# Performance work log

Hardware: AMD Instinct MI355X
Metric: run time of the kernel (lower is better)

Reference implementation:

```python
import jax, jax.numpy as jnp
import numpy as np

FPS = [32, 64, 128, 256]
SPATIAL = [(32, 32, 32), (16, 16, 16), (8, 8, 8), (4, 4, 4)]
N_FEAT = 512
B = 2
HEAD_DIM = 16
EPS = 1e-5


def setup_inputs() -> dict:
    key = jax.random.key(0)
    ks = iter(jax.random.split(key, 64))
    inp = {}
    for i, (c, (h, w, z)) in enumerate(zip(FPS, SPATIAL)):
        inp[f"x{i}"] = jax.random.normal(next(ks), (B, c, h, w, z), jnp.float32)
        inp[f"f{i}"] = jax.random.normal(next(ks), (N_FEAT, c), jnp.float32)
        inp[f"kv_w{i}"] = jax.random.normal(next(ks), (2 * c, c), jnp.float32) * 0.02
        inp[f"kv_b{i}"] = jnp.zeros((2 * c,), jnp.float32)
        inp[f"proj_w{i}"] = jax.random.normal(next(ks), (c, c), jnp.float32) * 0.02
        inp[f"proj_b{i}"] = jnp.zeros((c,), jnp.float32)
        inp[f"ln_g{i}"] = jnp.ones((c,), jnp.float32)
        inp[f"ln_b{i}"] = jnp.zeros((c,), jnp.float32)
    inp["x4"] = jax.random.normal(next(ks), (B, 320, 2, 2, 2), jnp.float32)
    inp["x5"] = jax.random.normal(next(ks), (B, 320, 1, 1, 1), jnp.float32)
    return inp


def _block(x5d, feat, kv_w, kv_b, proj_w, proj_b, ln_g, ln_b):
    b, c, h, w, z = x5d.shape
    n = h * w * z
    H = c // HEAD_DIM
    # torch's x.view(b, h*w*z, c) is a raw reshape of [b,c,h,w,z] memory
    xq = x5d.reshape(b, n, c)
    N = feat.shape[0]
    f = jnp.broadcast_to(feat[None], (b, N, c))
    kv = f @ kv_w.T + kv_b                     # [b, N, 2c]
    kv = kv.reshape(b, N, 2, H, HEAD_DIM)
    k = kv[:, :, 0].transpose(0, 2, 1, 3)      # [b, H, N, hd]
    v = kv[:, :, 1].transpose(0, 2, 1, 3)      # [b, H, N, hd]
    q = xq.reshape(b, n, H, HEAD_DIM).transpose(0, 2, 1, 3) * (HEAD_DIM ** -0.5)
    attn = jax.nn.softmax(jnp.einsum('bhnd,bhmd->bhnm', q, k), axis=-1)
    o = jnp.einsum('bhnm,bhmd->bhnd', attn, v)
    o = o.transpose(0, 2, 1, 3).reshape(b, n, c)
    o = o @ proj_w.T + proj_b
    y = 0.5 * o + 0.5 * xq
    mu = jnp.mean(y, axis=-1, keepdims=True)
    var = jnp.var(y, axis=-1, keepdims=True)
    y = (y - mu) / jnp.sqrt(var + EPS) * ln_g + ln_b
    return y.reshape(b, c, h, w, z)


def reference(x0, x1, x2, x3, x4, x5, f0, f1, f2, f3,
              kv_w0, kv_b0, proj_w0, proj_b0, ln_g0, ln_b0,
              kv_w1, kv_b1, proj_w1, proj_b1, ln_g1, ln_b1,
              kv_w2, kv_b2, proj_w2, proj_b2, ln_g2, ln_b2,
              kv_w3, kv_b3, proj_w3, proj_b3, ln_g3, ln_b3):
    xs = [x0, x1, x2, x3]
    fs = [f0, f1, f2, f3]
    ps = [(kv_w0, kv_b0, proj_w0, proj_b0, ln_g0, ln_b0),
          (kv_w1, kv_b1, proj_w1, proj_b1, ln_g1, ln_b1),
          (kv_w2, kv_b2, proj_w2, proj_b2, ln_g2, ln_b2),
          (kv_w3, kv_b3, proj_w3, proj_b3, ln_g3, ln_b3)]
    res = [_block(xs[i], fs[i], *ps[i]) for i in range(4)]
    res.append(x4)  # stage 4: i >= 4 -> passthrough
    res.append(x5)  # last stage appended as-is
    return tuple(res)
```

## Files before the change

### kernel.cpp

```cpp
#include <hip/hip_runtime.h>

#define LOG2E 1.44269504088896340736f

struct Params {
  const float* x[4]; const float* f[4]; const float* kvw[4]; const float* kvb[4];
  const float* pw[4]; const float* pb[4]; const float* g[4]; const float* lb[4];
  float* kb[4]; float* vb[4]; float* ob[4]; float* out[4];
};

__device__ inline float dot4(float4 a, float4 b) {
  return fmaf(a.w, b.w, fmaf(a.z, b.z, fmaf(a.y, b.y, a.x * b.x)));
}
__device__ inline void fma4(float4& a, float p, float4 v) {
  a.x = fmaf(p, v.x, a.x); a.y = fmaf(p, v.y, a.y);
  a.z = fmaf(p, v.z, a.z); a.w = fmaf(p, v.w, a.w);
}
__device__ inline void scale4(float4& a, float r) { a.x *= r; a.y *= r; a.z *= r; a.w *= r; }

__global__ __launch_bounds__(256) void kv_all(Params P) {
  int bid = blockIdx.x;
  int s, local;
  if (bid < 8)       { s = 0; local = bid; }
  else if (bid < 24) { s = 1; local = bid - 8; }
  else if (bid < 56) { s = 2; local = bid - 24; }
  else               { s = 3; local = bid - 56; }
  const int C = 32 << s;
  int nt = local & 7, jt = local >> 3;
  int n0 = nt * 64, j0 = jt * 64;
  const float* __restrict__ f = P.f[s];
  const float* __restrict__ w = P.kvw[s];
  __shared__ float fa[64][17];
  __shared__ float wb[64][17];
  int t = threadIdx.x;
  int ti = t & 15, tj = t >> 4;
  float acc[4][4];
  #pragma unroll
  for (int a = 0; a < 4; a++)
    #pragma unroll
    for (int b = 0; b < 4; b++) acc[a][b] = 0.f;

  for (int k0 = 0; k0 < C; k0 += 16) {
    __syncthreads();
    for (int i = t; i < 1024; i += 256) {
      int r = i >> 4, kk = i & 15;
      fa[r][kk] = f[(n0 + r) * C + k0 + kk];
      wb[r][kk] = w[(j0 + r) * C + k0 + kk];
    }
    __syncthreads();
    #pragma unroll
    for (int kk = 0; kk < 16; ++kk) {
      float av[4], bv[4];
      #pragma unroll
      for (int ii = 0; ii < 4; ii++) av[ii] = fa[ti * 4 + ii][kk];
      #pragma unroll
      for (int jj = 0; jj < 4; jj++) bv[jj] = wb[tj * 4 + jj][kk];
      #pragma unroll
      for (int ii = 0; ii < 4; ii++)
        #pragma unroll
        for (int jj = 0; jj < 4; jj++)
          acc[ii][jj] = fmaf(av[ii], bv[jj], acc[ii][jj]);
    }
  }
  const float* __restrict__ bias = P.kvb[s];
  float* kb = P.kb[s]; float* vb = P.vb[s];
  #pragma unroll
  for (int ii = 0; ii < 4; ii++) {
    int n = n0 + ti * 4 + ii;
    #pragma unroll
    for (int jj = 0; jj < 4; jj++) {
      int j = j0 + tj * 4 + jj;
      float val = acc[ii][jj] + bias[j];
      if (j < C) {
        kb[((j >> 4) * 512 + n) * 16 + (j & 15)] = val;
      } else {
        int j2 = j - C;
        vb[((j2 >> 4) * 512 + n) * 16 + (j2 & 15)] = val;
      }
    }
  }
}

template <int C, int H>
__device__ void attn_stage(const Params& P, int s, int local, float4* kvl) {
  constexpr int ROWS = 2 * ((C == 32) ? 32768 : (C == 64) ? 4096 : (C == 128) ? 512 : 64);
  int tile = local / H, head = local % H;
  const float4* __restrict__ kh = (const float4*)(P.kb[s] + head * 8192);
  const float4* __restrict__ vh = (const float4*)(P.vb[s] + head * 8192);
  int t = threadIdx.x;
  int row = tile * 256 + t;
  bool valid = row < ROWS;
  int rc = valid ? row : (ROWS - 1);

  const float* xr = P.x[s] + (size_t)rc * C + head * 16;
  float4 q0 = ((const float4*)xr)[0], q1 = ((const float4*)xr)[1],
         q2 = ((const float4*)xr)[2], q3 = ((const float4*)xr)[3];
  const float qs = 0.25f * LOG2E;
  scale4(q0, qs); scale4(q1, qs); scale4(q2, qs); scale4(q3, qs);

  float m = -1e30f, l = 0.f;
  float4 a0 = {0,0,0,0}, a1 = {0,0,0,0}, a2 = {0,0,0,0}, a3 = {0,0,0,0};

  float4 pk0 = kh[t], pk1 = kh[t + 256], pv0 = vh[t], pv1 = vh[t + 256];
  kvl[t] = pk0; kvl[t + 256] = pk1; kvl[512 + t] = pv0; kvl[512 + t + 256] = pv1;

  for (int c = 0; c < 4; ++c) {
    if (c < 3) {
      const float4* kp = kh + (c + 1) * 512;
      const float4* vp = vh + (c + 1) * 512;
      pk0 = kp[t]; pk1 = kp[t + 256]; pv0 = vp[t]; pv1 = vp[t + 256];
    }
    __syncthreads();
    #pragma unroll 2
    for (int key = 0; key < 128; ++key) {
      float4 k0 = kvl[key * 4 + 0], k1 = kvl[key * 4 + 1],
             k2 = kvl[key * 4 + 2], k3 = kvl[key * 4 + 3];
      float s0 = dot4(q0, k0), s1 = dot4(q1, k1), s2 = dot4(q2, k2), s3 = dot4(q3, k3);
      float sc = (s0 + s1) + (s2 + s3);
      if (__any(sc > m + 8.f)) {
        float mn = fmaxf(m, sc);
        float r = __builtin_amdgcn_exp2f(m - mn);
        l *= r;
        scale4(a0, r); scale4(a1, r); scale4(a2, r); scale4(a3, r);
        m = mn;
      }
      float p = __builtin_amdgcn_exp2f(sc - m);
      l += p;
      float4 v0 = kvl[512 + key * 4 + 0], v1 = kvl[512 + key * 4 + 1],
             v2 = kvl[512 + key * 4 + 2], v3 = kvl[512 + key * 4 + 3];
      fma4(a0, p, v0); fma4(a1, p, v1); fma4(a2, p, v2); fma4(a3, p, v3);
    }
    __syncthreads();
    if (c < 3) {
      kvl[t] = pk0; kvl[t + 256] = pk1; kvl[512 + t] = pv0; kvl[512 + t + 256] = pv1;
    }
  }
  if (valid) {
    float inv = 1.f / l;
    scale4(a0, inv); scale4(a1, inv); scale4(a2, inv); scale4(a3, inv);
    float* orow = P.ob[s] + (size_t)row * C + head * 16;
    ((float4*)orow)[0] = a0; ((float4*)orow)[1] = a1;
    ((float4*)orow)[2] = a2; ((float4*)orow)[3] = a3;
  }
}

__global__ __launch_bounds__(256, 4) void attn_all(Params P) {
  __shared__ float4 kvlds[1024];
  int bid = blockIdx.x;
  if (bid < 512)      attn_stage<32, 2>(P, 0, bid, kvlds);
  else if (bid < 640) attn_stage<64, 4>(P, 1, bid - 512, kvlds);
  else if (bid < 672) attn_stage<128, 8>(P, 2, bid - 640, kvlds);
  else                attn_stage<256, 16>(P, 3, bid - 672, kvlds);
}

template <int C>
__device__ void proj_stage(const Params& P, int s, int tile, float* olds) {
  constexpr int CP = C + 4;
  constexpr int R = 256 / C;
  constexpr int NR = 8;
  constexpr int RB = 2048 / C;
  int r0 = tile * RB;
  int t = threadIdx.x;
  const float4* __restrict__ obv = (const float4*)(P.ob[s] + (size_t)r0 * C);
  for (int i = t; i < 512; i += 256) {
    int row = i / (C / 4), kk = i % (C / 4);
    ((float4*)(olds + row * CP))[kk] = obv[i];
  }
  __syncthreads();
  int j = t % C, rg = t / C;
  const float* __restrict__ pw = P.pw[s];
  float acc[NR];
  #pragma unroll
  for (int i = 0; i < NR; ++i) acc[i] = 0.f;
  for (int k = 0; k < C; k += 4) {
    float4 w4 = *(const float4*)(pw + (size_t)j * C + k);
    #pragma unroll
    for (int i = 0; i < NR; ++i) {
      float4 o4 = *(const float4*)(olds + (rg + i * R) * CP + k);
      acc[i] = fmaf(o4.x, w4.x, acc[i]);
      acc[i] = fmaf(o4.y, w4.y, acc[i]);
      acc[i] = fmaf(o4.z, w4.z, acc[i]);
      acc[i] = fmaf(o4.w, w4.w, acc[i]);
    }
  }
  __syncthreads();
  float pbj = P.pb[s][j];
  const float* __restrict__ x = P.x[s];
  #pragma unroll
  for (int i = 0; i < NR; ++i) {
    int r = rg + i * R;
    float xv = x[(size_t)(r0 + r) * C + j];
    olds[r * CP + j] = 0.5f * (acc[i] + pbj) + 0.5f * xv;
  }
  __syncthreads();
  int lane = t & 63, wv = t >> 6;
  const float* __restrict__ g = P.g[s];
  const float* __restrict__ lb = P.lb[s];
  float* __restrict__ out = P.out[s];
  #pragma unroll
  for (int rr = 0; rr < RB / 4; ++rr) {
    int r = wv * (RB / 4) + rr;
    float sum = 0.f, sq = 0.f;
    #pragma unroll
    for (int ch = lane; ch < C; ch += 64) {
      float v = olds[r * CP + ch];
      sum += v; sq = fmaf(v, v, sq);
    }
    #pragma unroll
    for (int o = 32; o; o >>= 1) { sum += __shfl_xor(sum, o); sq += __shfl_xor(sq, o); }
    float mu = sum * (1.f / C);
    float var = sq * (1.f / C) - mu * mu;
    float rstd = rsqrtf(var + 1e-5f);
    #pragma unroll
    for (int ch = lane; ch < C; ch += 64) {
      float v = (olds[r * CP + ch] - mu) * rstd;
      out[(size_t)(r0 + r) * C + ch] = fmaf(v, g[ch], lb[ch]);
    }
  }
}

__global__ __launch_bounds__(256) void proj_ln_all(Params P) {
  __shared__ float olds[2304];
  int bid = blockIdx.x;
  if (bid < 1024)      proj_stage<32>(P, 0, bid, olds);
  else if (bid < 1280) proj_stage<64>(P, 1, bid - 1024, olds);
  else if (bid < 1344) proj_stage<128>(P, 2, bid - 1280, olds);
  else                 proj_stage<256>(P, 3, bid - 1344, olds);
}

extern "C" void kernel_launch(void* const* d_in, const int* in_sizes, int n_in,
                              void* d_out, int out_size, void* d_ws, size_t ws_size,
                              hipStream_t stream) {
  Params P;
  float* ws = (float*)d_ws;
  float* out = (float*)d_out;
  const size_t kvoff[4]  = {0, 32768, 98304, 229376};
  const size_t ksz[4]    = {16384, 32768, 65536, 131072};
  const size_t ooff[4]   = {491520, 2588672, 3112960, 3244032};
  const size_t outoff[4] = {0, 2097152, 2621440, 2752512};
  for (int i = 0; i < 4; ++i) {
    const int b = i * 8;
    P.x[i]   = (const float*)d_in[b + 0];
    P.f[i]   = (const float*)d_in[b + 1];
    P.kvw[i] = (const float*)d_in[b + 2];
    P.kvb[i] = (const float*)d_in[b + 3];
    P.pw[i]  = (const float*)d_in[b + 4];
    P.pb[i]  = (const float*)d_in[b + 5];
    P.g[i]   = (const float*)d_in[b + 6];
    P.lb[i]  = (const float*)d_in[b + 7];
    P.kb[i]  = ws + kvoff[i];
    P.vb[i]  = ws + kvoff[i] + ksz[i];
    P.ob[i]  = ws + ooff[i];
    P.out[i] = out + outoff[i];
  }
  hipMemcpyAsync(out + 2785280, d_in[32], 5120 * sizeof(float), hipMemcpyDeviceToDevice, stream);
  hipMemcpyAsync(out + 2790400, d_in[33], 640 * sizeof(float), hipMemcpyDeviceToDevice, stream);

  kv_all<<<120, 256, 0, stream>>>(P);
  attn_all<<<688, 256, 0, stream>>>(P);
  proj_ln_all<<<1360, 256, 0, stream>>>(P);
}
```

Measured before the change: 355.1 us.

## Process two query rows per thread with interleaved K/V layout in attention

The attention kernel now runs 128 threads per block, with each thread handling two query rows (row and row+128). Every K/V value read from shared memory is therefore reused for two rows. K and V are written interleaved per key (32 floats per key), so one shared-memory row holds both, and the math uses native vector types. The two memcpy calls for the passthrough tensors become one small copy kernel, saving an API call and a launch. In exchange, each thread holds more registers, there are fewer waves per block, and the online-softmax rescale is now evaluated jointly for both rows.

```diff
diff --git a/kernel.cpp b/kernel.cpp
--- a/kernel.cpp
+++ b/kernel.cpp
@@ -1,21 +1,16 @@
 #include <hip/hip_runtime.h>
 
 #define LOG2E 1.44269504088896340736f
+
+typedef float v4f __attribute__((ext_vector_type(4)));
 
 struct Params {
   const float* x[4]; const float* f[4]; const float* kvw[4]; const float* kvb[4];
   const float* pw[4]; const float* pb[4]; const float* g[4]; const float* lb[4];
-  float* kb[4]; float* vb[4]; float* ob[4]; float* out[4];
+  float* kb[4]; float* ob[4]; float* out[4];
 };
 
-__device__ inline float dot4(float4 a, float4 b) {
-  return fmaf(a.w, b.w, fmaf(a.z, b.z, fmaf(a.y, b.y, a.x * b.x)));
-}
-__device__ inline void fma4(float4& a, float p, float4 v) {
-  a.x = fmaf(p, v.x, a.x); a.y = fmaf(p, v.y, a.y);
-  a.z = fmaf(p, v.z, a.z); a.w = fmaf(p, v.w, a.w);
-}
-__device__ inline void scale4(float4& a, float r) { a.x *= r; a.y *= r; a.z *= r; a.w *= r; }
+__device__ inline v4f fmav(v4f a, v4f b, v4f c) { return a * b + c; }
 
 __global__ __launch_bounds__(256) void kv_all(Params P) {
   int bid = blockIdx.x;
@@ -62,7 +57,7 @@
     }
   }
   const float* __restrict__ bias = P.kvb[s];
-  float* kb = P.kb[s]; float* vb = P.vb[s];
+  float* kb = P.kb[s];
   #pragma unroll
   for (int ii = 0; ii < 4; ii++) {
     int n = n0 + ti * 4 + ii;
@@ -71,85 +66,106 @@
       int j = j0 + tj * 4 + jj;
       float val = acc[ii][jj] + bias[j];
       if (j < C) {
-        kb[((j >> 4) * 512 + n) * 16 + (j & 15)] = val;
+        kb[(j >> 4) * 16384 + n * 32 + (j & 15)] = val;
       } else {
         int j2 = j - C;
-        vb[((j2 >> 4) * 512 + n) * 16 + (j2 & 15)] = val;
+        kb[(j2 >> 4) * 16384 + n * 32 + 16 + (j2 & 15)] = val;
       }
     }
   }
 }
 
 template <int C, int H>
-__device__ void attn_stage(const Params& P, int s, int local, float4* kvl) {
+__device__ void attn_stage(const Params& P, int s, int local, v4f* kvl) {
   constexpr int ROWS = 2 * ((C == 32) ? 32768 : (C == 64) ? 4096 : (C == 128) ? 512 : 64);
   int tile = local / H, head = local % H;
-  const float4* __restrict__ kh = (const float4*)(P.kb[s] + head * 8192);
-  const float4* __restrict__ vh = (const float4*)(P.vb[s] + head * 8192);
+  const v4f* __restrict__ kvh = (const v4f*)(P.kb[s] + head * 16384);
   int t = threadIdx.x;
-  int row = tile * 256 + t;
-  bool valid = row < ROWS;
-  int rc = valid ? row : (ROWS - 1);
-
-  const float* xr = P.x[s] + (size_t)rc * C + head * 16;
-  float4 q0 = ((const float4*)xr)[0], q1 = ((const float4*)xr)[1],
-         q2 = ((const float4*)xr)[2], q3 = ((const float4*)xr)[3];
+  int rowA = tile * 256 + t, rowB = rowA + 128;
+  bool vA = rowA < ROWS, vB = rowB < ROWS;
+  int rA = vA ? rowA : (ROWS - 1), rB = vB ? rowB : (ROWS - 1);
+
+  const v4f* xa = (const v4f*)(P.x[s] + (size_t)rA * C + head * 16);
+  const v4f* xb = (const v4f*)(P.x[s] + (size_t)rB * C + head * 16);
   const float qs = 0.25f * LOG2E;
-  scale4(q0, qs); scale4(q1, qs); scale4(q2, qs); scale4(q3, qs);
-
-  float m = -1e30f, l = 0.f;
-  float4 a0 = {0,0,0,0}, a1 = {0,0,0,0}, a2 = {0,0,0,0}, a3 = {0,0,0,0};
-
-  float4 pk0 = kh[t], pk1 = kh[t + 256], pv0 = vh[t], pv1 = vh[t + 256];
-  kvl[t] = pk0; kvl[t + 256] = pk1; kvl[512 + t] = pv0; kvl[512 + t + 256] = pv1;
+  v4f qa0 = xa[0] * qs, qa1 = xa[1] * qs, qa2 = xa[2] * qs, qa3 = xa[3] * qs;
+  v4f qb0 = xb[0] * qs, qb1 = xb[1] * qs, qb2 = xb[2] * qs, qb3 = xb[3] * qs;
+
+  float ma = -1e30f, la = 0.f, mb = -1e30f, lb = 0.f;
+  v4f aa0 = 0.f, aa1 = 0.f, aa2 = 0.f, aa3 = 0.f;
+  v4f ab0 = 0.f, ab1 = 0.f, ab2 = 0.f, ab3 = 0.f;
+
+  v4f pk[8];
+  #pragma unroll
+  for (int j = 0; j < 8; ++j) pk[j] = kvh[t + 128 * j];
+  #pragma unroll
+  for (int j = 0; j < 8; ++j) kvl[t + 128 * j] = pk[j];
 
   for (int c = 0; c < 4; ++c) {
     if (c < 3) {
-      const float4* kp = kh + (c + 1) * 512;
-      const float4* vp = vh + (c + 1) * 512;
-      pk0 = kp[t]; pk1 = kp[t + 256]; pv0 = vp[t]; pv1 = vp[t + 256];
+      const v4f* src = kvh + (c + 1) * 1024;
+      #pragma unroll
+      for (int j = 0; j < 8; ++j) pk[j] = src[t + 128 * j];
     }
     __syncthreads();
     #pragma unroll 2
-    for (int key = 0; key < 128; ++key) {
-      float4 k0 = kvl[key * 4 + 0], k1 = kvl[key * 4 + 1],
-             k2 = kvl[key * 4 + 2], k3 = kvl[key * 4 + 3];
-      float s0 = dot4(q0, k0), s1 = dot4(q1, k1), s2 = dot4(q2, k2), s3 = dot4(q3, k3);
-      float sc = (s0 + s1) + (s2 + s3);
-      if (__any(sc > m + 8.f)) {
-        float mn = fmaxf(m, sc);
-        float r = __builtin_amdgcn_exp2f(m - mn);
-        l *= r;
-        scale4(a0, r); scale4(a1, r); scale4(a2, r); scale4(a3, r);
-        m = mn;
+    for (int kl = 0; kl < 128; ++kl) {
+      const v4f* row = kvl + kl * 8;
+      v4f k0 = row[0], k1 = row[1], k2 = row[2], k3 = row[3];
+      v4f ta = qa0 * k0; ta = fmav(qa1, k1, ta); ta = fmav(qa2, k2, ta); ta = fmav(qa3, k3, ta);
+      v4f tb = qb0 * k0; tb = fmav(qb1, k1, tb); tb = fmav(qb2, k2, tb); tb = fmav(qb3, k3, tb);
+      float sa = (ta.x + ta.y) + (ta.z + ta.w);
+      float sb = (tb.x + tb.y) + (tb.z + tb.w);
+      if (__any(fmaxf(sa - ma, sb - mb) > 8.f)) {
+        float mna = fmaxf(ma, sa);
+        float ra = __builtin_amdgcn_exp2f(ma - mna);
+        la *= ra; aa0 *= ra; aa1 *= ra; aa2 *= ra; aa3 *= ra; ma = mna;
+        float mnb = fmaxf(mb, sb);
+        float rb = __builtin_amdgcn_exp2f(mb - mnb);
+        lb *= rb; ab0 *= rb; ab1 *= rb; ab2 *= rb; ab3 *= rb; mb = mnb;
       }
-      float p = __builtin_amdgcn_exp2f(sc - m);
-      l += p;
-      float4 v0 = kvl[512 + key * 4 + 0], v1 = kvl[512 + key * 4 + 1],
-             v2 = kvl[512 + key * 4 + 2], v3 = kvl[512 + key * 4 + 3];
-      fma4(a0, p, v0); fma4(a1, p, v1); fma4(a2, p, v2); fma4(a3, p, v3);
+      float pa = __builtin_amdgcn_exp2f(sa - ma);
+      float pb = __builtin_amdgcn_exp2f(sb - mb);
+      la += pa; lb += pb;
+      v4f v0 = row[4], v1 = row[5], v2 = row[6], v3 = row[7];
+      aa0 = fmav(pa, v0, aa0); aa1 = fmav(pa, v1, aa1);
+      aa2 = fmav(pa, v2, aa2); aa3 = fmav(pa, v3, aa3);
+      ab0 = fmav(pb, v0, ab0); ab1 = fmav(pb, v1, ab1);
+      ab2 = fmav(pb, v2, ab2); ab3 = fmav(pb, v3, ab3);
     }
     __syncthreads();
     if (c < 3) {
-      kvl[t] = pk0; kvl[t + 256] = pk1; kvl[512 + t] = pv0; kvl[512 + t + 256] = pv1;
-    }
-  }
-  if (valid) {
-    float inv = 1.f / l;
-    scale4(a0, inv); scale4(a1, inv); scale4(a2, inv); scale4(a3, inv);
-    float* orow = P.ob[s] + (size_t)row * C + head * 16;
-    ((float4*)orow)[0] = a0; ((float4*)orow)[1] = a1;
-    ((float4*)orow)[2] = a2; ((float4*)orow)[3] = a3;
-  }
-}
-
-__global__ __launch_bounds__(256, 4) void attn_all(Params P) {
-  __shared__ float4 kvlds[1024];
+      #pragma unroll
+      for (int j = 0; j < 8; ++j) kvl[t + 128 * j] = pk[j];
+    }
+  }
+  if (vA) {
+    float inv = 1.f / la;
+    v4f* o = (v4f*)(P.ob[s] + (size_t)rowA * C + head * 16);
+    o[0] = aa0 * inv; o[1] = aa1 * inv; o[2] = aa2 * inv; o[3] = aa3 * inv;
+  }
+  if (vB) {
+    float inv = 1.f / lb;
+    v4f* o = (v4f*)(P.ob[s] + (size_t)rowB * C + head * 16);
+    o[0] = ab0 * inv; o[1] = ab1 * inv; o[2] = ab2 * inv; o[3] = ab3 * inv;
+  }
+}
+
+__global__ __launch_bounds__(128) void attn_all(Params P) {
+  __shared__ v4f kvlds[1024];
   int bid = blockIdx.x;
   if (bid < 512)      attn_stage<32, 2>(P, 0, bid, kvlds);
   else if (bid < 640) attn_stage<64, 4>(P, 1, bid - 512, kvlds);
   else if (bid < 672) attn_stage<128, 8>(P, 2, bid - 640, kvlds);
   else                attn_stage<256, 16>(P, 3, bid - 672, kvlds);
+}
+
+__global__ __launch_bounds__(256) void copy_pass(const float4* __restrict__ x4,
+                                                 const float4* __restrict__ x5,
+                                                 float4* __restrict__ o) {
+  int i = blockIdx.x * 256 + threadIdx.x;
+  if (i < 1280)      o[i] = x4[i];
+  else if (i < 1440) o[i] = x5[i - 1280];
 }
 
 template <int C>
@@ -234,7 +250,6 @@
   float* ws = (float*)d_ws;
   float* out = (float*)d_out;
   const size_t kvoff[4]  = {0, 32768, 98304, 229376};
-  const size_t ksz[4]    = {16384, 32768, 65536, 131072};
   const size_t ooff[4]   = {491520, 2588672, 3112960, 3244032};
   const size_t outoff[4] = {0, 2097152, 2621440, 2752512};
   for (int i = 0; i < 4; ++i) {
@@ -248,14 +263,13 @@
     P.g[i]   = (const float*)d_in[b + 6];
     P.lb[i]  = (const float*)d_in[b + 7];
     P.kb[i]  = ws + kvoff[i];
-    P.vb[i]  = ws + kvoff[i] + ksz[i];
     P.ob[i]  = ws + ooff[i];
     P.out[i] = out + outoff[i];
   }
-  hipMemcpyAsync(out + 2785280, d_in[32], 5120 * sizeof(float), hipMemcpyDeviceToDevice, stream);
-  hipMemcpyAsync(out + 2790400, d_in[33], 640 * sizeof(float), hipMemcpyDeviceToDevice, stream);
-
+
+  copy_pass<<<6, 256, 0, stream>>>((const float4*)d_in[32], (const float4*)d_in[33],
+                                   (float4*)(out + 2785280));
   kv_all<<<120, 256, 0, stream>>>(P);
-  attn_all<<<688, 256, 0, stream>>>(P);
+  attn_all<<<688, 128, 0, stream>>>(P);
   proj_ln_all<<<1360, 256, 0, stream>>>(P);
 }
```

Result: faster. 318.4 us (-10.4%).

## Interleave K/V rows and read keys directly from global memory instead of LDS

Applied to the files above, without the earlier changes.

The KV projection now writes K and V interleaved per key (32 floats per key per head), so the attention kernel can read each key's K and V contiguously. The attention loop drops the LDS staging and double-buffer synchronisation. Each thread now loads uniform K/V addresses straight from global memory, relying on the cache and broadcast. It also replaces the two device-to-device memcpys with a small copy kernel and uses native vector types. The risk is higher global/L1 load latency per key in exchange for removing barriers and LDS traffic.

```diff
diff --git a/kernel.cpp b/kernel.cpp
--- a/kernel.cpp
+++ b/kernel.cpp
@@ -1,21 +1,16 @@
 #include <hip/hip_runtime.h>
 
 #define LOG2E 1.44269504088896340736f
+
+typedef float v4f __attribute__((ext_vector_type(4)));
 
 struct Params {
   const float* x[4]; const float* f[4]; const float* kvw[4]; const float* kvb[4];
   const float* pw[4]; const float* pb[4]; const float* g[4]; const float* lb[4];
-  float* kb[4]; float* vb[4]; float* ob[4]; float* out[4];
+  float* kb[4]; float* ob[4]; float* out[4];
 };
 
-__device__ inline float dot4(float4 a, float4 b) {
-  return fmaf(a.w, b.w, fmaf(a.z, b.z, fmaf(a.y, b.y, a.x * b.x)));
-}
-__device__ inline void fma4(float4& a, float p, float4 v) {
-  a.x = fmaf(p, v.x, a.x); a.y = fmaf(p, v.y, a.y);
-  a.z = fmaf(p, v.z, a.z); a.w = fmaf(p, v.w, a.w);
-}
-__device__ inline void scale4(float4& a, float r) { a.x *= r; a.y *= r; a.z *= r; a.w *= r; }
+__device__ inline v4f fmav(v4f a, v4f b, v4f c) { return a * b + c; }
 
 __global__ __launch_bounds__(256) void kv_all(Params P) {
   int bid = blockIdx.x;
@@ -62,7 +57,7 @@
     }
   }
   const float* __restrict__ bias = P.kvb[s];
-  float* kb = P.kb[s]; float* vb = P.vb[s];
+  float* kb = P.kb[s];
   #pragma unroll
   for (int ii = 0; ii < 4; ii++) {
     int n = n0 + ti * 4 + ii;
@@ -71,85 +66,78 @@
       int j = j0 + tj * 4 + jj;
       float val = acc[ii][jj] + bias[j];
       if (j < C) {
-        kb[((j >> 4) * 512 + n) * 16 + (j & 15)] = val;
+        kb[(j >> 4) * 16384 + n * 32 + (j & 15)] = val;
       } else {
         int j2 = j - C;
-        vb[((j2 >> 4) * 512 + n) * 16 + (j2 & 15)] = val;
+        kb[(j2 >> 4) * 16384 + n * 32 + 16 + (j2 & 15)] = val;
       }
     }
   }
 }
 
 template <int C, int H>
-__device__ void attn_stage(const Params& P, int s, int local, float4* kvl) {
+__device__ void attn_stage(const float* __restrict__ kb, const float* __restrict__ x,
+                           float* __restrict__ ob, int local) {
   constexpr int ROWS = 2 * ((C == 32) ? 32768 : (C == 64) ? 4096 : (C == 128) ? 512 : 64);
   int tile = local / H, head = local % H;
-  const float4* __restrict__ kh = (const float4*)(P.kb[s] + head * 8192);
-  const float4* __restrict__ vh = (const float4*)(P.vb[s] + head * 8192);
+  const float* __restrict__ kvh = kb + head * 16384;
   int t = threadIdx.x;
   int row = tile * 256 + t;
   bool valid = row < ROWS;
   int rc = valid ? row : (ROWS - 1);
 
-  const float* xr = P.x[s] + (size_t)rc * C + head * 16;
-  float4 q0 = ((const float4*)xr)[0], q1 = ((const float4*)xr)[1],
-         q2 = ((const float4*)xr)[2], q3 = ((const float4*)xr)[3];
+  const v4f* xr = (const v4f*)(x + (size_t)rc * C + head * 16);
   const float qs = 0.25f * LOG2E;
-  scale4(q0, qs); scale4(q1, qs); scale4(q2, qs); scale4(q3, qs);
+  v4f q0 = xr[0] * qs, q1 = xr[1] * qs, q2 = xr[2] * qs, q3 = xr[3] * qs;
 
   float m = -1e30f, l = 0.f;
-  float4 a0 = {0,0,0,0}, a1 = {0,0,0,0}, a2 = {0,0,0,0}, a3 = {0,0,0,0};
-
-  float4 pk0 = kh[t], pk1 = kh[t + 256], pv0 = vh[t], pv1 = vh[t + 256];
-  kvl[t] = pk0; kvl[t + 256] = pk1; kvl[512 + t] = pv0; kvl[512 + t + 256] = pv1;
-
-  for (int c = 0; c < 4; ++c) {
-    if (c < 3) {
-      const float4* kp = kh + (c + 1) * 512;
-      const float4* vp = vh + (c + 1) * 512;
-      pk0 = kp[t]; pk1 = kp[t + 256]; pv0 = vp[t]; pv1 = vp[t + 256];
-    }
-    __syncthreads();
-    #pragma unroll 2
-    for (int key = 0; key < 128; ++key) {
-      float4 k0 = kvl[key * 4 + 0], k1 = kvl[key * 4 + 1],
-             k2 = kvl[key * 4 + 2], k3 = kvl[key * 4 + 3];
-      float s0 = dot4(q0, k0), s1 = dot4(q1, k1), s2 = dot4(q2, k2), s3 = dot4(q3, k3);
-      float sc = (s0 + s1) + (s2 + s3);
-      if (__any(sc > m + 8.f)) {
-        float mn = fmaxf(m, sc);
-        float r = __builtin_amdgcn_exp2f(m - mn);
-        l *= r;
-        scale4(a0, r); scale4(a1, r); scale4(a2, r); scale4(a3, r);
-        m = mn;
-      }
-      float p = __builtin_amdgcn_exp2f(sc - m);
-      l += p;
-      float4 v0 = kvl[512 + key * 4 + 0], v1 = kvl[512 + key * 4 + 1],
-             v2 = kvl[512 + key * 4 + 2], v3 = kvl[512 + key * 4 + 3];
-      fma4(a0, p, v0); fma4(a1, p, v1); fma4(a2, p, v2); fma4(a3, p, v3);
-    }
-    __syncthreads();
-    if (c < 3) {
-      kvl[t] = pk0; kvl[t + 256] = pk1; kvl[512 + t] = pv0; kvl[512 + t + 256] = pv1;
-    }
-  }
+  v4f a0 = 0.f, a1 = 0.f, a2 = 0.f, a3 = 0.f;
+
+  #pragma unroll 2
+  for (int key = 0; key < 512; ++key) {
+    const v4f* kr = (const v4f*)(kvh + key * 32);
+    v4f k0 = kr[0], k1 = kr[1], k2 = kr[2], k3 = kr[3];
+    v4f tv = q0 * k0; tv = fmav(q1, k1, tv); tv = fmav(q2, k2, tv); tv = fmav(q3, k3, tv);
+    float sc = (tv.x + tv.y) + (tv.z + tv.w);
+    if (__any(sc > m + 8.f)) {
+      float mn = fmaxf(m, sc);
+      float r = __builtin_amdgcn_exp2f(m - mn);
+      l *= r; a0 *= r; a1 *= r; a2 *= r; a3 *= r; m = mn;
+    }
+    float p = __builtin_amdgcn_exp2f(sc - m);
+    l += p;
+    v4f v0 = kr[4], v1 = kr[5], v2 = kr[6], v3 = kr[7];
+    a0 = fmav(p, v0, a0); a1 = fmav(p, v1, a1);
+    a2 = fmav(p, v2, a2); a3 = fmav(p, v3, a3);
+  }
+
   if (valid) {
     float inv = 1.f / l;
-    scale4(a0, inv); scale4(a1, inv); scale4(a2, inv); scale4(a3, inv);
-    float* orow = P.ob[s] + (size_t)row * C + head * 16;
-    ((float4*)orow)[0] = a0; ((float4*)orow)[1] = a1;
-    ((float4*)orow)[2] = a2; ((float4*)orow)[3] = a3;
-  }
-}
-
-__global__ __launch_bounds__(256, 4) void attn_all(Params P) {
-  __shared__ float4 kvlds[1024];
+    v4f* o = (v4f*)(ob + (size_t)row * C + head * 16);
+    o[0] = a0 * inv; o[1] = a1 * inv; o[2] = a2 * inv; o[3] = a3 * inv;
+  }
+}
+
+__global__ __launch_bounds__(256) void attn_all(
+    const float* __restrict__ kb0, const float* __restrict__ kb1,
+    const float* __restrict__ kb2, const float* __restrict__ kb3,
+    const float* __restrict__ x0, const float* __restrict__ x1,
+    const float* __restrict__ x2, const float* __restrict__ x3,
+    float* __restrict__ ob0, float* __restrict__ ob1,
+    float* __restrict__ ob2, float* __restrict__ ob3) {
   int bid = blockIdx.x;
-  if (bid < 512)      attn_stage<32, 2>(P, 0, bid, kvlds);
-  else if (bid < 640) attn_stage<64, 4>(P, 1, bid - 512, kvlds);
-  else if (bid < 672) attn_stage<128, 8>(P, 2, bid - 640, kvlds);
-  else                attn_stage<256, 16>(P, 3, bid - 672, kvlds);
+  if (bid < 512)      attn_stage<32, 2>(kb0, x0, ob0, bid);
+  else if (bid < 640) attn_stage<64, 4>(kb1, x1, ob1, bid - 512);
+  else if (bid < 672) attn_stage<128, 8>(kb2, x2, ob2, bid - 640);
+  else                attn_stage<256, 16>(kb3, x3, ob3, bid - 672);
+}
+
+__global__ __launch_bounds__(256) void copy_pass(const float4* __restrict__ x4,
+                                                 const float4* __restrict__ x5,
+                                                 float4* __restrict__ o) {
+  int i = blockIdx.x * 256 + threadIdx.x;
+  if (i < 1280)      o[i] = x4[i];
+  else if (i < 1440) o[i] = x5[i - 1280];
 }
 
 template <int C>
@@ -234,7 +222,6 @@
   float* ws = (float*)d_ws;
   float* out = (float*)d_out;
   const size_t kvoff[4]  = {0, 32768, 98304, 229376};
-  const size_t ksz[4]    = {16384, 32768, 65536, 131072};
   const size_t ooff[4]   = {491520, 2588672, 3112960, 3244032};
   const size_t outoff[4] = {0, 2097152, 2621440, 2752512};
   for (int i = 0; i < 4; ++i) {
@@ -248,14 +235,15 @@
     P.g[i]   = (const float*)d_in[b + 6];
     P.lb[i]  = (const float*)d_in[b + 7];
     P.kb[i]  = ws + kvoff[i];
-    P.vb[i]  = ws + kvoff[i] + ksz[i];
     P.ob[i]  = ws + ooff[i];
     P.out[i] = out + outoff[i];
   }
-  hipMemcpyAsync(out + 2785280, d_in[32], 5120 * sizeof(float), hipMemcpyDeviceToDevice, stream);
-  hipMemcpyAsync(out + 2790400, d_in[33], 640 * sizeof(float), hipMemcpyDeviceToDevice, stream);
-
+
+  copy_pass<<<6, 256, 0, stream>>>((const float4*)d_in[32], (const float4*)d_in[33],
+                                   (float4*)(out + 2785280));
   kv_all<<<120, 256, 0, stream>>>(P);
-  attn_all<<<688, 256, 0, stream>>>(P);
+  attn_all<<<688, 256, 0, stream>>>(P.kb[0], P.kb[1], P.kb[2], P.kb[3],
+                                    P.x[0], P.x[1], P.x[2], P.x[3],
+                                    P.ob[0], P.ob[1], P.ob[2], P.ob[3]);
   proj_ln_all<<<1360, 256, 0, stream>>>(P);
 }
```

Result: slower. 420.5 us (+18.4%).
